# Optimization experiments

Measured on AMD Instinct MI355X. Metric: run time of the kernel, lower is better.

Reference implementation:

```python
import jax, jax.numpy as jnp
import numpy as np

FEAT = 32      # feature_dim
NA = 64        # num_azimuths
NE = 32        # num_elevations - 2 (interior elevation rings)
N = 2_000_000  # number of query points
NORMALIZED = False


def setup_inputs() -> dict:
    key = jax.random.key(0)
    k1, k2, k3 = jax.random.split(key, 3)
    u = jax.random.uniform(k1, (2, N), dtype=jnp.float32)
    # azimuth in [-pi, pi), elevation in [-pi/2, pi/2]
    az = u[0] * (2.0 * np.pi) * (1.0 - 1e-7) - np.pi
    el = u[1] * np.pi - np.pi / 2
    points_to_interp = jnp.stack([az, el])
    grid_values = jax.random.normal(k2, (FEAT, NA, NE), dtype=jnp.float32) * 0.1
    grid_values_poles = jax.random.normal(k3, (FEAT, 2), dtype=jnp.float32) * 0.1
    return {
        "points_to_interp": points_to_interp,
        "grid_values": grid_values,
        "grid_values_poles": grid_values_poles,
    }


def _slerp(f1, f2, theta, omega, normalized):
    # spherical linear interpolation weights; omega is a static python float
    w1 = jnp.sin(omega - theta)
    w2 = jnp.sin(theta)
    if normalized:
        s = w1 + w2
        w1 = w1 / s
        w2 = w2 / s
    else:
        so = np.sin(omega)
        w1 = w1 / so
        w2 = w2 / so
    return w1 * f1 + w2 * f2


def reference(points_to_interp, grid_values, grid_values_poles):
    F, na, ne = grid_values.shape
    # static grid ticks (buffers in the torch module)
    ticks_az = jnp.asarray(np.linspace(-np.pi, np.pi, na + 1)[:-1], jnp.float32)
    ticks_el = jnp.asarray(np.linspace(-np.pi / 2, np.pi / 2, ne + 2)[1:-1], jnp.float32)
    omega_az = 2.0 * np.pi / na            # azimuth tick spacing
    omega_el = np.pi / (ne + 1)            # elevation tick spacing (incl. poles)

    az = points_to_interp[0]
    el = points_to_interp[1]

    # torch.bucketize(right=False) == searchsorted side='left'
    ar = jnp.searchsorted(ticks_az, az, side="left")
    al = ar - 1
    ar = jnp.where(ar >= na, 0, ar)        # azimuth wraps around
    al = jnp.where(al < 0, na - 1, al)     # torch negative index wrap

    er = jnp.searchsorted(ticks_el, el, side="left")
    south = er == 0                        # below lowest interior ring
    north = er == ne                       # above highest interior ring
    eil = jnp.clip(er - 1, 0, ne - 1)      # lower ring index (clamped)
    eir = jnp.clip(er, 0, ne - 1)          # upper ring index (clamped)

    # azimuth slerp on the lower and upper rings (4 gathers of [F, N])
    theta_az = az - ticks_az[al]
    f_b = _slerp(grid_values[:, al, eil], grid_values[:, ar, eil], theta_az, omega_az, NORMALIZED)
    f_t = _slerp(grid_values[:, al, eir], grid_values[:, ar, eir], theta_az, omega_az, NORMALIZED)

    # pole regions: blend ring value with pole feature.
    # slerp(a, b, theta, omega) == slerp(b, a, omega - theta, omega), so the
    # north-pole branch slerp(pole, f_top_ring, pi/2 - el) equals
    # slerp(f_top_ring, pole, el - ticks_el[ne-1]) with the same omega_el.
    f1 = jnp.where(south, grid_values_poles[:, 0:1], f_b)
    f2 = jnp.where(north, grid_values_poles[:, 1:2], f_t)
    base = jnp.where(south, -np.pi / 2, ticks_el[eil])
    theta_el = el - base
    return _slerp(f1, f2, theta_el, omega_el, NORMALIZED)
```

## Files before the change

### kernel.cpp

```cpp
#include <hip/hip_runtime.h>
#include <hip/hip_fp16.h>

namespace {

constexpr int kFeat = 32;
constexpr int kNA = 64;
constexpr int kNE = 32;
constexpr int kGridElems = kFeat * kNA * kNE;
constexpr int kPoleElems = kFeat * 2;
constexpr int kCols = kNA * kNE;
constexpr int kColS = kCols;
constexpr int kColN = kCols + 1;
constexpr int kTotCols = kCols + 2;

constexpr float kPi  = 3.14159265358979323846f;
constexpr float kPi2 = 1.57079632679489661923f;
constexpr float kOmegaAz = 0.09817477042468103f;
constexpr float kOmegaEl = 0.09519977738150889f;
constexpr float kInvOmegaAz = 10.18591635788130f;
constexpr float kInvOmegaEl = 10.50422624406509f;
constexpr float kInvSinAz = 10.20229703f;
constexpr float kInvSinEl = 10.52010966f;

__global__ __launch_bounds__(256) void transpose_grid_h(
    const float* __restrict__ g, const float* __restrict__ poles,
    __half* __restrict__ gt) {
  int idx = blockIdx.x * 256 + threadIdx.x;
  if (idx < kGridElems) {
    int f = idx >> 11;
    int ae = idx & 2047;
    gt[ae * kFeat + f] = __float2half(g[idx]);
  }
  if (idx < kPoleElems) {
    int f = idx >> 1;
    int p = idx & 1;
    gt[(kCols + p) * kFeat + f] = __float2half(poles[idx]);
  }
}

struct PointSetup {
  int col_bl, col_br, col_tl, col_tr;
  float a1, a2, b1, b2;
};

__device__ __forceinline__ PointSetup setup_point(float az, float el) {
  PointSetup s;
  float ta = (az + kPi) * kInvOmegaAz;
  int ar0 = (int)ceilf(ta);
  int al = ar0 - 1;
  int ar = (ar0 >= kNA) ? 0 : ar0;
  if (al < 0) al = kNA - 1;
  float theta_a = az - (-kPi + (float)al * kOmegaAz);
  float w1a = __sinf(kOmegaAz - theta_a) * kInvSinAz;
  float w2a = __sinf(theta_a) * kInvSinAz;

  float ue = (el + kPi2) * kInvOmegaEl;
  int er = (int)ceilf(ue) - 1;
  er = min(max(er, 0), kNE);
  bool south = (er == 0);
  bool north = (er == kNE);
  int eil = min(max(er - 1, 0), kNE - 1);
  int eir = min(er, kNE - 1);
  float base = south ? -kPi2 : (-kPi2 + (float)(eil + 1) * kOmegaEl);
  float theta_e = el - base;
  float w1e = __sinf(kOmegaEl - theta_e) * kInvSinEl;
  float w2e = __sinf(theta_e) * kInvSinEl;

  s.col_bl = al * kNE + eil;
  s.col_br = ar * kNE + eil;
  s.col_tl = al * kNE + eir;
  s.col_tr = ar * kNE + eir;
  s.a1 = w1e * w1a; s.a2 = w1e * w2a;
  s.b1 = w2e * w1a; s.b2 = w2e * w2a;
  if (south) {
    s.col_bl = kColS; s.col_br = kColS;
    s.a1 = 0.5f * w1e; s.a2 = s.a1;
  }
  if (north) {
    s.col_tl = kColN; s.col_tr = kColN;
    s.b1 = 0.5f * w2e; s.b2 = s.b1;
  }
  return s;
}

constexpr int kTile = 256;
constexpr int kTileFloats = kFeat * kTile;

__global__ __launch_bounds__(256) void interp_o(
    const float* __restrict__ pts, const __half* __restrict__ gt,
    float* __restrict__ out, int n) {
  __shared__ float tile[kTileFloats];
  const int base = blockIdx.x * kTile;
  const int rem = min(kTile, n - base);
  const size_t sn = (size_t)n;
  const int t = threadIdx.x;

  if (t < rem) {
    const int i = base + t;
    const float az = pts[i];
    const float el = pts[n + i];
    PointSetup s = setup_point(az, el);

    const uint4* cbl = (const uint4*)(gt + s.col_bl * kFeat);
    const uint4* cbr = (const uint4*)(gt + s.col_br * kFeat);
    const uint4* ctl = (const uint4*)(gt + s.col_tl * kFeat);
    const uint4* ctr = (const uint4*)(gt + s.col_tr * kFeat);

    union H8 { uint4 u; __half2 h[4]; };
    H8 bl[4], br[4], tl[4], tr[4];
#pragma unroll
    for (int q = 0; q < 4; ++q) {
      bl[q].u = cbl[q];
      br[q].u = cbr[q];
      tl[q].u = ctl[q];
      tr[q].u = ctr[q];
    }

#pragma unroll
    for (int q = 0; q < 4; ++q) {
#pragma unroll
      for (int h = 0; h < 4; ++h) {
        float2 vbl = __half22float2(bl[q].h[h]);
        float2 vbr = __half22float2(br[q].h[h]);
        float2 vtl = __half22float2(tl[q].h[h]);
        float2 vtr = __half22float2(tr[q].h[h]);
        const int f = 8 * q + 2 * h;
        tile[(f + 0) * kTile + t] =
            s.a1 * vbl.x + s.a2 * vbr.x + s.b1 * vtl.x + s.b2 * vtr.x;
        tile[(f + 1) * kTile + t] =
            s.a1 * vbl.y + s.a2 * vbr.y + s.b1 * vtl.y + s.b2 * vtr.y;
      }
    }
  }

  __syncthreads();

  if (rem == kTile) {
#pragma unroll
    for (int r = 0; r < 8; ++r) {
      int u = t + 256 * r;
      int row = u >> 6;
      int c4 = (u & 63) * 4;
      uint4 v = *(const uint4*)(tile + row * kTile + c4);
      *(uint4*)(out + (size_t)row * sn + base + c4) = v;
    }
  } else {
    for (int r = 0; r < 8; ++r) {
      int u = t + 256 * r;
      int row = u >> 6;
      int c4 = (u & 63) * 4;
      float* o = out + (size_t)row * sn + base;
      for (int e = 0; e < 4; ++e) {
        int p = c4 + e;
        if (p < rem) o[p] = tile[row * kTile + p];
      }
    }
  }
}

__global__ __launch_bounds__(256) void interp_d(
    const float* __restrict__ pts, const float* __restrict__ g,
    const float* __restrict__ poles, float* __restrict__ out, int n) {
  int i = blockIdx.x * 256 + threadIdx.x;
  if (i >= n) return;
  float az = pts[i];
  float el = pts[n + i];
  PointSetup s = setup_point(az, el);

  float a1 = s.a1, a2 = s.a2, b1 = s.b1, b2 = s.b2;
  float pw0 = 0.0f, pw1 = 0.0f;
  if (s.col_bl == kColS) { pw0 = a1 + a2; a1 = 0.0f; a2 = 0.0f; }
  if (s.col_tl == kColN) { pw1 = b1 + b2; b1 = 0.0f; b2 = 0.0f; }

  const float* gbl = g + (s.col_bl < kCols ? s.col_bl : 0);
  const float* gbr = g + (s.col_br < kCols ? s.col_br : 0);
  const float* gtl = g + (s.col_tl < kCols ? s.col_tl : 0);
  const float* gtr = g + (s.col_tr < kCols ? s.col_tr : 0);
  size_t sn = (size_t)n;
#pragma unroll 8
  for (int f = 0; f < kFeat; ++f) {
    float v = a1 * gbl[f * kCols] + a2 * gbr[f * kCols]
            + b1 * gtl[f * kCols] + b2 * gtr[f * kCols]
            + pw0 * poles[f * 2 + 0] + pw1 * poles[f * 2 + 1];
    out[(size_t)f * sn + i] = v;
  }
}

}

extern "C" void kernel_launch(void* const* d_in, const int* in_sizes, int n_in,
                              void* d_out, int out_size, void* d_ws, size_t ws_size,
                              hipStream_t stream) {
  (void)n_in; (void)out_size;
  const float* pts   = (const float*)d_in[0];
  const float* grid  = (const float*)d_in[1];
  const float* poles = (const float*)d_in[2];
  float* out = (float*)d_out;
  int n = in_sizes[0] / 2;

  size_t need = (size_t)(kTotCols * kFeat) * sizeof(__half);
  if (ws_size >= need) {
    __half* gt = (__half*)d_ws;
    transpose_grid_h<<<(kGridElems + 255) / 256, 256, 0, stream>>>(grid, poles, gt);
    int blocks = (n + kTile - 1) / kTile;
    interp_o<<<blocks, 256, 0, stream>>>(pts, gt, out, n);
  } else {
    int blocks = (n + 255) / 256;
    interp_d<<<blocks, 256, 0, stream>>>(pts, grid, poles, out, n);
  }
}
```

Before: 314.1 us.

## Split each point's gather across four lanes using wave shuffles

```diff
diff --git a/kernel.cpp b/kernel.cpp
--- a/kernel.cpp
+++ b/kernel.cpp
@@ -86,7 +86,7 @@
 constexpr int kTile = 256;
 constexpr int kTileFloats = kFeat * kTile;
 
-__global__ __launch_bounds__(256) void interp_o(
+__global__ __launch_bounds__(256) void interp_s(
     const float* __restrict__ pts, const __half* __restrict__ gt,
     float* __restrict__ out, int n) {
   __shared__ float tile[kTileFloats];
@@ -94,41 +94,48 @@
   const int rem = min(kTile, n - base);
   const size_t sn = (size_t)n;
   const int t = threadIdx.x;
-
-  if (t < rem) {
-    const int i = base + t;
-    const float az = pts[i];
-    const float el = pts[n + i];
-    PointSetup s = setup_point(az, el);
-
-    const uint4* cbl = (const uint4*)(gt + s.col_bl * kFeat);
-    const uint4* cbr = (const uint4*)(gt + s.col_br * kFeat);
-    const uint4* ctl = (const uint4*)(gt + s.col_tl * kFeat);
-    const uint4* ctr = (const uint4*)(gt + s.col_tr * kFeat);
-
-    union H8 { uint4 u; __half2 h[4]; };
-    H8 bl[4], br[4], tl[4], tr[4];
+  const int w = t >> 6;
+  const int l = t & 63;
+
+  const int p_own = w * 16 + 64 * (l >> 4) + (l & 15);
+  const int pc = min(p_own, rem - 1);
+  const float az = pts[base + pc];
+  const float el = pts[n + base + pc];
+  const PointSetup so = setup_point(az, el);
+
+  const int j = l & 3;
+  const int off = j * 8;
+
 #pragma unroll
-    for (int q = 0; q < 4; ++q) {
-      bl[q].u = cbl[q];
-      br[q].u = cbr[q];
-      tl[q].u = ctl[q];
-      tr[q].u = ctr[q];
-    }
-
+  for (int c = 0; c < 4; ++c) {
+    const int src = c * 16 + (l >> 2);
+    const int cbl = __shfl(so.col_bl, src);
+    const int cbr = __shfl(so.col_br, src);
+    const int ctl = __shfl(so.col_tl, src);
+    const int ctr = __shfl(so.col_tr, src);
+    const float a1 = __shfl(so.a1, src);
+    const float a2 = __shfl(so.a2, src);
+    const float b1 = __shfl(so.b1, src);
+    const float b2 = __shfl(so.b2, src);
+    const int p = w * 16 + 64 * c + (l >> 2);
+    if (p < rem) {
+      union H8 { uint4 u; __half2 h[4]; };
+      H8 bl, br, tl, tr;
+      bl.u = *(const uint4*)(gt + cbl * kFeat + off);
+      br.u = *(const uint4*)(gt + cbr * kFeat + off);
+      tl.u = *(const uint4*)(gt + ctl * kFeat + off);
+      tr.u = *(const uint4*)(gt + ctr * kFeat + off);
+      float* dst = tile + (8 * j) * kTile + p;
 #pragma unroll
-    for (int q = 0; q < 4; ++q) {
-#pragma unroll
-      for (int h = 0; h < 4; ++h) {
-        float2 vbl = __half22float2(bl[q].h[h]);
-        float2 vbr = __half22float2(br[q].h[h]);
-        float2 vtl = __half22float2(tl[q].h[h]);
-        float2 vtr = __half22float2(tr[q].h[h]);
-        const int f = 8 * q + 2 * h;
-        tile[(f + 0) * kTile + t] =
-            s.a1 * vbl.x + s.a2 * vbr.x + s.b1 * vtl.x + s.b2 * vtr.x;
-        tile[(f + 1) * kTile + t] =
-            s.a1 * vbl.y + s.a2 * vbr.y + s.b1 * vtl.y + s.b2 * vtr.y;
+      for (int q = 0; q < 4; ++q) {
+        float2 vbl = __half22float2(bl.h[q]);
+        float2 vbr = __half22float2(br.h[q]);
+        float2 vtl = __half22float2(tl.h[q]);
+        float2 vtr = __half22float2(tr.h[q]);
+        dst[(2 * q + 0) * kTile] =
+            a1 * vbl.x + a2 * vbr.x + b1 * vtl.x + b2 * vtr.x;
+        dst[(2 * q + 1) * kTile] =
+            a1 * vbl.y + a2 * vbr.y + b1 * vtl.y + b2 * vtr.y;
       }
     }
   }
@@ -203,7 +210,7 @@
     __half* gt = (__half*)d_ws;
     transpose_grid_h<<<(kGridElems + 255) / 256, 256, 0, stream>>>(grid, poles, gt);
     int blocks = (n + kTile - 1) / kTile;
-    interp_o<<<blocks, 256, 0, stream>>>(pts, gt, out, n);
+    interp_s<<<blocks, 256, 0, stream>>>(pts, gt, out, n);
   } else {
     int blocks = (n + 255) / 256;
     interp_d<<<blocks, 256, 0, stream>>>(pts, grid, poles, out, n);
```

New measurement: 285.1 us. 1.1x faster.
